# Optimization experiments

Hardware: AMD Instinct MI355X
Metric: run time of the kernel (lower is better)

## Reference

```python
import jax, jax.numpy as jnp
import numpy as np
import math

B, T, D = 1, 4096, 1024
H = 16
HD = D // H  # 64


def _rotate_half(x):
    d = x.shape[-1] // 2
    return jnp.concatenate([-x[..., d:], x[..., :d]], axis=-1)


def setup_inputs() -> dict:
    key = jax.random.key(0)
    k1, k2, k3 = jax.random.split(key, 3)
    x = jax.random.normal(k1, (B, T, D), dtype=jnp.float32)
    # Linear weights stored as (in, out) so forward is x @ W
    w_qkv = jax.random.normal(k2, (D, 3 * D), dtype=jnp.float32) * (1.0 / math.sqrt(D))
    w_proj = jax.random.normal(k3, (D, D), dtype=jnp.float32) * (1.0 / math.sqrt(D))
    return {"x": x, "w_qkv": w_qkv, "w_proj": w_proj}


def reference(x, w_qkv, w_proj):
    b, t, c = x.shape
    qkv = x @ w_qkv  # [b,t,3c]
    q, k, v = jnp.split(qkv, 3, axis=-1)
    # [b,h,t,hd]
    q = q.reshape(b, t, H, HD).transpose(0, 2, 1, 3)
    k = k.reshape(b, t, H, HD).transpose(0, 2, 1, 3)
    v = v.reshape(b, t, H, HD).transpose(0, 2, 1, 3)

    # RoPE (rotate_half style)
    inv_freq = 1.0 / (10000.0 ** (jnp.arange(0, HD, 2, dtype=jnp.float32) / HD))
    pos = jnp.arange(t, dtype=jnp.float32)
    freqs = jnp.outer(pos, inv_freq)            # [t, hd/2]
    cos = jnp.concatenate([jnp.cos(freqs), jnp.cos(freqs)], axis=-1)[None, None]  # [1,1,t,hd]
    sin = jnp.concatenate([jnp.sin(freqs), jnp.sin(freqs)], axis=-1)[None, None]
    q = q * cos + _rotate_half(q) * sin
    k = k * cos + _rotate_half(k) * sin

    att = jnp.einsum('bhqd,bhkd->bhqk', q, k) / math.sqrt(HD)  # [b,h,t,t]
    causal = jnp.tril(jnp.ones((t, t), dtype=bool))
    att = jnp.where(causal, att, -jnp.inf)
    att = jax.nn.softmax(att, axis=-1)
    # dropout is identity in eval mode
    y = jnp.einsum('bhqk,bhkd->bhqd', att, v)
    y = y.transpose(0, 2, 1, 3).reshape(b, t, c)
    return y @ w_proj
```

## Files before the change

kernel.cpp:

```cpp
#include <hip/hip_runtime.h>
#include <math.h>

#define TT 4096
#define DD 1024
#define NH 16
#define HD 64

typedef __attribute__((ext_vector_type(8))) _Float16 half8v;
typedef __attribute__((ext_vector_type(4))) _Float16 half4v;
typedef __attribute__((ext_vector_type(4))) float f32x4;

#define GLDS16(g, l)                                                        \
    __builtin_amdgcn_global_load_lds(                                       \
        (const __attribute__((address_space(1))) void*)(g),                 \
        (__attribute__((address_space(3))) void*)(l), 16, 0, 0)

__global__ __launch_bounds__(256) void cast_x(const float* __restrict__ X,
                                              _Float16* __restrict__ Xh)
{
    const int i = (blockIdx.x * 256 + threadIdx.x) * 8;
    float4 a = *(const float4*)&X[i];
    float4 b = *(const float4*)&X[i + 4];
    half8v o = {(_Float16)a.x, (_Float16)a.y, (_Float16)a.z, (_Float16)a.w,
                (_Float16)b.x, (_Float16)b.y, (_Float16)b.z, (_Float16)b.w};
    *(half8v*)&Xh[i] = o;
}

__global__ __launch_bounds__(256) void transpose_cast(
    const float* __restrict__ W, _Float16* __restrict__ WT, int K, int N)
{
    __shared__ float tile[64][65];
    const int t = threadIdx.x;
    const int k0 = blockIdx.y * 64, n0 = blockIdx.x * 64;
    const int c = (t & 15) * 4, r = t >> 4;
#pragma unroll
    for (int i = 0; i < 4; i++) {
        float4 v = *(const float4*)&W[(size_t)(k0 + r + 16 * i) * N + n0 + c];
        tile[r + 16 * i][c + 0] = v.x;
        tile[r + 16 * i][c + 1] = v.y;
        tile[r + 16 * i][c + 2] = v.z;
        tile[r + 16 * i][c + 3] = v.w;
    }
    __syncthreads();
#pragma unroll
    for (int i = 0; i < 4; i++) {
        const int n = r + 16 * i;
        half4v o;
        o[0] = (_Float16)tile[c + 0][n];
        o[1] = (_Float16)tile[c + 1][n];
        o[2] = (_Float16)tile[c + 2][n];
        o[3] = (_Float16)tile[c + 3][n];
        *(half4v*)&WT[(size_t)(n0 + n) * K + k0 + c] = o;
    }
}

template <int MODE>
__global__ __launch_bounds__(256) void gemm_h(
    const _Float16* __restrict__ A, const _Float16* __restrict__ Bt,
    float* __restrict__ C0, _Float16* __restrict__ Q,
    _Float16* __restrict__ Kk, _Float16* __restrict__ V,
    int M, int N, int K)
{
    __shared__ _Float16 As[128 * 32];
    __shared__ _Float16 Bs[128 * 32];
    const int tid  = threadIdx.x;
    const int wave = tid >> 6;
    const int lane = tid & 63;
    const int quad = lane >> 4;
    const int n16  = lane & 15;
    const int n0 = blockIdx.x * 128;
    const int m0 = blockIdx.y * 128;
    const int wr = (wave & 1) * 64;
    const int wc = (wave >> 1) * 64;

    f32x4 acc[4][4];
#pragma unroll
    for (int i = 0; i < 4; i++)
#pragma unroll
        for (int j = 0; j < 4; j++) acc[i][j] = (f32x4){0.f, 0.f, 0.f, 0.f};

    const int srow = tid >> 2;
    const int scol = (tid & 3) * 8;
    const _Float16* Ag = A + (size_t)(m0 + srow) * K + scol;
    const _Float16* Bg = Bt + (size_t)(n0 + srow) * K + scol;
    _Float16* AsW = As + (size_t)wave * 512;
    _Float16* BsW = Bs + (size_t)wave * 512;

    for (int k0 = 0; k0 < K; k0 += 32) {
        __syncthreads();
        GLDS16(Ag + k0, AsW);
        GLDS16(Ag + (size_t)64 * K + k0, AsW + 2048);
        GLDS16(Bg + k0, BsW);
        GLDS16(Bg + (size_t)64 * K + k0, BsW + 2048);
        __syncthreads();

        half8v aF[4], bF[4];
#pragma unroll
        for (int i = 0; i < 4; i++)
            aF[i] = *(const half8v*)&As[(size_t)(wr + i * 16 + n16) * 32 + quad * 8];
#pragma unroll
        for (int j = 0; j < 4; j++)
            bF[j] = *(const half8v*)&Bs[(size_t)(wc + j * 16 + n16) * 32 + quad * 8];
#pragma unroll
        for (int i = 0; i < 4; i++)
#pragma unroll
            for (int j = 0; j < 4; j++)
                acc[i][j] = __builtin_amdgcn_mfma_f32_16x16x32_f16(
                    aF[i], bF[j], acc[i][j], 0, 0, 0);
    }

#pragma unroll
    for (int i = 0; i < 4; i++) {
#pragma unroll
        for (int j = 0; j < 4; j++) {
#pragma unroll
            for (int r = 0; r < 4; r++) {
                const int m = m0 + wr + i * 16 + quad * 4 + r;
                const int n = n0 + wc + j * 16 + n16;
                const float val = acc[i][j][r];
                if (MODE == 0) {
                    C0[(size_t)m * N + n] = val;
                } else {
                    const int which = n >> 10;
                    const int col = n & 1023;
                    const int h = col >> 6, d = col & 63;
                    const size_t off = ((size_t)h * TT + m) * HD + d;
                    if (which == 0) Q[off] = (_Float16)val;
                    else if (which == 1) Kk[off] = (_Float16)val;
                    else V[off] = (_Float16)val;
                }
            }
        }
    }
}

__global__ __launch_bounds__(256) void rope_h(_Float16* __restrict__ Q,
                                              _Float16* __restrict__ Kb)
{
    const int idx = blockIdx.x * 256 + threadIdx.x;
    const int i = idx & 31;
    const int t = (idx >> 5) & (TT - 1);
    const int h = idx >> 17;
    if (h >= NH) return;

    const float inv = expf(-(float)i * (logf(10000.0f) / 32.0f));
    const float f = (float)t * inv;
    const float c = cosf(f), s = sinf(f);
    const size_t base = ((size_t)h * TT + t) * HD + i;
    const float QS = 0.125f * 1.44269504f;

    float q1 = (float)Q[base], q2 = (float)Q[base + 32];
    Q[base]      = (_Float16)((q1 * c - q2 * s) * QS);
    Q[base + 32] = (_Float16)((q2 * c + q1 * s) * QS);
    float k1 = (float)Kb[base], k2 = (float)Kb[base + 32];
    Kb[base]      = (_Float16)(k1 * c - k2 * s);
    Kb[base + 32] = (_Float16)(k2 * c + k1 * s);
}

__global__ __launch_bounds__(256) void transpose_v(
    const _Float16* __restrict__ V, _Float16* __restrict__ Vt)
{
    __shared__ _Float16 tile[256][72];
    const int h = blockIdx.y;
    const int t0 = blockIdx.x * 256;
    const int tid = threadIdx.x;
    const _Float16* Vg = V + (size_t)h * TT * HD;
    _Float16* Vo = Vt + (size_t)h * TT * HD;

#pragma unroll
    for (int i = 0; i < 4; i++) {
        const int chunk = tid + 256 * i;
        const int row = chunk >> 2, c = (chunk & 3) * 16;
        half8v v0 = *(const half8v*)(Vg + (size_t)(t0 + row) * HD + c);
        half8v v1 = *(const half8v*)(Vg + (size_t)(t0 + row) * HD + c + 8);
        *(half8v*)&tile[row][c] = v0;
        *(half8v*)&tile[row][c + 8] = v1;
    }
    __syncthreads();

    const int s = tid & 15;
#pragma unroll
    for (int dd = 0; dd < 4; ++dd) {
        const int d = dd * 16 + (tid >> 4);
        half8v o0, o1;
#pragma unroll
        for (int e = 0; e < 8; e++) o0[e] = tile[s * 16 + e][d];
#pragma unroll
        for (int e = 0; e < 8; e++) o1[e] = tile[s * 16 + 8 + e][d];
        *(half8v*)(Vo + (size_t)d * TT + t0 + s * 16) = o0;
        *(half8v*)(Vo + (size_t)d * TT + t0 + s * 16 + 8) = o1;
    }
}

__global__ __launch_bounds__(256) void attn_kernel(
    const _Float16* __restrict__ Qh, const _Float16* __restrict__ Kh,
    const _Float16* __restrict__ Vt, _Float16* __restrict__ Y)
{
    __shared__ _Float16 Ks[2][32][32];
    __shared__ _Float16 Vs[64][32];
    __shared__ _Float16 Ps[4][32][32];

    const int tid  = threadIdx.x;
    const int wave = tid >> 6;
    const int lane = tid & 63;
    const int quad = lane >> 4;
    const int n16  = lane & 15;
    const int h  = blockIdx.y;
    const int qt = gridDim.x - 1 - blockIdx.x;
    const int q0 = qt * 128;
    const int rowbase = q0 + wave * 32;

    const _Float16* Qg = Qh + (size_t)h * TT * HD;
    const _Float16* Kg = Kh + (size_t)h * TT * HD;
    const _Float16* Vg = Vt + (size_t)h * TT * HD;

    half8v aQ[2][2];
#pragma unroll
    for (int g = 0; g < 2; g++) {
        const int row = rowbase + g * 16 + n16;
#pragma unroll
        for (int c = 0; c < 2; c++)
            aQ[g][c] = *(const half8v*)(Qg + (size_t)row * HD + c * 32 + quad * 8);
    }

    f32x4 O[2][4];
#pragma unroll
    for (int g = 0; g < 2; g++)
#pragma unroll
        for (int d = 0; d < 4; d++) O[g][d] = (f32x4){0.f, 0.f, 0.f, 0.f};
    float l[2][4] = {{0.f, 0.f, 0.f, 0.f}, {0.f, 0.f, 0.f, 0.f}};

    const int kc = tid >> 7, kj = (tid >> 2) & 31, ks = tid & 3;
    const _Float16* kSrc = Kg + (size_t)kj * HD + kc * 32 + ks * 8;
    const int vd = tid >> 2, vs = tid & 3;
    const _Float16* vSrc = Vg + (size_t)vd * TT + vs * 8;
    _Float16* ksBase = &Ks[0][0][0] + (size_t)wave * 512;
    _Float16* vsBase = &Vs[0][0] + (size_t)wave * 512;

    const int nTiles = qt * 4 + 4;

    for (int it = 0; it < nTiles; ++it) {
        const int j0 = it * 32;
        __syncthreads();
        GLDS16(kSrc + (size_t)j0 * HD, ksBase);
        GLDS16(vSrc + j0, vsBase);
        __syncthreads();

        if (j0 <= rowbase + 31) {
            const bool needMask = (j0 + 31 > rowbase);

            f32x4 S[2][2];
#pragma unroll
            for (int g = 0; g < 2; g++)
#pragma unroll
                for (int st = 0; st < 2; st++) {
                    S[g][st] = (f32x4){0.f, 0.f, 0.f, 0.f};
#pragma unroll
                    for (int c = 0; c < 2; c++) {
                        half8v bK = *(const half8v*)&Ks[c][st * 16 + n16][quad * 8];
                        S[g][st] = __builtin_amdgcn_mfma_f32_16x16x32_f16(
                            aQ[g][c], bK, S[g][st], 0, 0, 0);
                    }
                }

#pragma unroll
            for (int g = 0; g < 2; g++)
#pragma unroll
                for (int r = 0; r < 4; r++) {
                    const int row = rowbase + g * 16 + quad * 4 + r;
                    float x0 = S[g][0][r];
                    float x1 = S[g][1][r];
                    if (needMask) {
                        x0 = (j0 + n16      <= row) ? x0 : -1e30f;
                        x1 = (j0 + 16 + n16 <= row) ? x1 : -1e30f;
                    }
                    const float p0 = __builtin_amdgcn_exp2f(x0);
                    const float p1 = __builtin_amdgcn_exp2f(x1);
                    l[g][r] += p0 + p1;
                    Ps[wave][g * 16 + quad * 4 + r][n16]      = (_Float16)p0;
                    Ps[wave][g * 16 + quad * 4 + r][16 + n16] = (_Float16)p1;
                }

            half8v bV[4];
#pragma unroll
            for (int d = 0; d < 4; d++)
                bV[d] = *(const half8v*)&Vs[d * 16 + n16][quad * 8];
#pragma unroll
            for (int g = 0; g < 2; g++) {
                half8v aP = *(const half8v*)&Ps[wave][g * 16 + n16][quad * 8];
#pragma unroll
                for (int d = 0; d < 4; d++)
                    O[g][d] = __builtin_amdgcn_mfma_f32_16x16x32_f16(
                        aP, bV[d], O[g][d], 0, 0, 0);
            }
        }
    }

#pragma unroll
    for (int g = 0; g < 2; g++)
#pragma unroll
        for (int r = 0; r < 4; r++) {
            float s = l[g][r];
            s += __shfl_xor(s, 1);
            s += __shfl_xor(s, 2);
            s += __shfl_xor(s, 4);
            s += __shfl_xor(s, 8);
            const float inv = 1.0f / s;
            const int row = rowbase + g * 16 + quad * 4 + r;
            _Float16* yrow = Y + (size_t)row * DD + h * HD;
#pragma unroll
            for (int d = 0; d < 4; d++)
                yrow[d * 16 + n16] = (_Float16)(O[g][d][r] * inv);
        }
}

extern "C" void kernel_launch(void* const* d_in, const int* in_sizes, int n_in,
                              void* d_out, int out_size, void* d_ws, size_t ws_size,
                              hipStream_t stream)
{
    const float* x      = (const float*)d_in[0];
    const float* w_qkv  = (const float*)d_in[1];
    const float* w_proj = (const float*)d_in[2];
    float* out = (float*)d_out;

    char* ws = (char*)d_ws;
    const size_t MB = 1u << 20;
    _Float16* xh  = (_Float16*)(ws);
    _Float16* WqT = (_Float16*)(ws + 8 * MB);
    _Float16* WpT = (_Float16*)(ws + 14 * MB);
    _Float16* Qh  = (_Float16*)(ws + 16 * MB);
    _Float16* Kh  = (_Float16*)(ws + 24 * MB);
    _Float16* Vh  = (_Float16*)(ws + 32 * MB);
    _Float16* Vtg = (_Float16*)(ws + 40 * MB);
    _Float16* Yh  = (_Float16*)(ws + 48 * MB);

    dim3 blk(256);

    cast_x<<<(TT * DD) / (256 * 8), blk, 0, stream>>>(x, xh);
    transpose_cast<<<dim3(3072 / 64, DD / 64), blk, 0, stream>>>(w_qkv, WqT, DD, 3 * DD);
    transpose_cast<<<dim3(DD / 64, DD / 64), blk, 0, stream>>>(w_proj, WpT, DD, DD);

    gemm_h<1><<<dim3(3072 / 128, TT / 128), blk, 0, stream>>>(
        xh, WqT, nullptr, Qh, Kh, Vh, TT, 3 * DD, DD);

    rope_h<<<(NH * TT * 32) / 256, blk, 0, stream>>>(Qh, Kh);
    transpose_v<<<dim3(TT / 256, NH), blk, 0, stream>>>(Vh, Vtg);

    attn_kernel<<<dim3(TT / 128, NH), blk, 0, stream>>>(Qh, Kh, Vtg, Yh);

    gemm_h<0><<<dim3(DD / 128, TT / 128), blk, 0, stream>>>(
        Yh, WpT, out, nullptr, nullptr, nullptr, TT, DD, DD);
}
```

Before: 312.1 us.

## Split causal attention over key ranges with atomic partial accumulation and finalize pass

Attention for each query tile is now split across up to four blocks, each covering a contiguous range of key tiles. The split count grows with the tile's causal length, which evens out per-block work and gives the GPU more blocks. Each block atomically adds its unnormalized fp16 output and fp32 row sums into zeroed buffers, and a separate finalize kernel divides by the sums. V is repacked into a per-32-key tile layout with interleaved keys so each tile loads contiguously, and P is written to a padded LDS array as half2 stores. The cost is two extra kernels, atomic traffic, and fp16 accumulation of unnormalized partial outputs, which risks precision loss or overflow.

```diff
diff --git a/kernel.cpp b/kernel.cpp
--- a/kernel.cpp
+++ b/kernel.cpp
@@ -1,4 +1,5 @@
 #include <hip/hip_runtime.h>
+#include <hip/hip_fp16.h>
 #include <math.h>
 
 #define TT 4096
@@ -158,14 +159,13 @@
 }
 
 __global__ __launch_bounds__(256) void transpose_v(
-    const _Float16* __restrict__ V, _Float16* __restrict__ Vt)
+    const _Float16* __restrict__ V, _Float16* __restrict__ Vp)
 {
     __shared__ _Float16 tile[256][72];
     const int h = blockIdx.y;
     const int t0 = blockIdx.x * 256;
     const int tid = threadIdx.x;
     const _Float16* Vg = V + (size_t)h * TT * HD;
-    _Float16* Vo = Vt + (size_t)h * TT * HD;
 
 #pragma unroll
     for (int i = 0; i < 4; i++) {
@@ -178,41 +178,62 @@
     }
     __syncthreads();
 
-    const int s = tid & 15;
-#pragma unroll
-    for (int dd = 0; dd < 4; ++dd) {
-        const int d = dd * 16 + (tid >> 4);
-        half8v o0, o1;
-#pragma unroll
-        for (int e = 0; e < 8; e++) o0[e] = tile[s * 16 + e][d];
-#pragma unroll
-        for (int e = 0; e < 8; e++) o1[e] = tile[s * 16 + 8 + e][d];
-        *(half8v*)(Vo + (size_t)d * TT + t0 + s * 16) = o0;
-        *(half8v*)(Vo + (size_t)d * TT + t0 + s * 16 + 8) = o1;
-    }
+    _Float16* Vo = Vp + ((size_t)h * (TT / 32) + (t0 >> 5)) * 64 * 32;
+#pragma unroll
+    for (int i = 0; i < 8; i++) {
+        const int item = tid + 256 * i;
+        const int cc = (item & 3) * 8;
+        const int d = (item >> 2) & 63;
+        const int kbl = item >> 8;
+        half8v o;
+#pragma unroll
+        for (int e = 0; e < 8; e++) {
+            const int cp = cc + e;
+            const int key = (cp >> 1) + 16 * (cp & 1);
+            o[e] = tile[kbl * 32 + key][d];
+        }
+        *(half8v*)(Vo + ((size_t)kbl * 64 + d) * 32 + cc) = o;
+    }
+}
+
+__global__ __launch_bounds__(256) void zero_acc(float4* __restrict__ O4,
+                                                float4* __restrict__ L4)
+{
+    const int i = blockIdx.x * 256 + threadIdx.x;
+    const float4 z = {0.f, 0.f, 0.f, 0.f};
+    O4[i] = z;
+    if (i < 16384) L4[i] = z;
 }
 
 __global__ __launch_bounds__(256) void attn_kernel(
     const _Float16* __restrict__ Qh, const _Float16* __restrict__ Kh,
-    const _Float16* __restrict__ Vt, _Float16* __restrict__ Y)
+    const _Float16* __restrict__ Vp, _Float16* __restrict__ Oacc,
+    float* __restrict__ Lacc)
 {
     __shared__ _Float16 Ks[2][32][32];
     __shared__ _Float16 Vs[64][32];
-    __shared__ _Float16 Ps[4][32][32];
+    __shared__ _Float16 Ps[4][32][40];
 
     const int tid  = threadIdx.x;
     const int wave = tid >> 6;
     const int lane = tid & 63;
     const int quad = lane >> 4;
     const int n16  = lane & 15;
-    const int h  = blockIdx.y;
-    const int qt = gridDim.x - 1 - blockIdx.x;
+    const int h  = blockIdx.z;
+    const int qt = 31 - blockIdx.y;
+    const int s  = blockIdx.x;
+    const int nT = 4 * qt + 4;
+    const int nS = (qt + 8) >> 3;
+    if (s >= nS) return;
+    const int t_beg = s * nT / nS;
+    const int t_end = (s + 1) * nT / nS;
+
     const int q0 = qt * 128;
     const int rowbase = q0 + wave * 32;
 
     const _Float16* Qg = Qh + (size_t)h * TT * HD;
     const _Float16* Kg = Kh + (size_t)h * TT * HD;
-    const _Float16* Vg = Vt + (size_t)h * TT * HD;
+    const _Float16* Vg = Vp + (size_t)h * (TT / 32) * 64 * 32;
 
     half8v aQ[2][2];
 #pragma unroll
@@ -232,18 +253,15 @@
 
     const int kc = tid >> 7, kj = (tid >> 2) & 31, ks = tid & 3;
     const _Float16* kSrc = Kg + (size_t)kj * HD + kc * 32 + ks * 8;
-    const int vd = tid >> 2, vs = tid & 3;
-    const _Float16* vSrc = Vg + (size_t)vd * TT + vs * 8;
+    const _Float16* vSrc = Vg + (size_t)tid * 8;
     _Float16* ksBase = &Ks[0][0][0] + (size_t)wave * 512;
     _Float16* vsBase = &Vs[0][0] + (size_t)wave * 512;
 
-    const int nTiles = qt * 4 + 4;
-
-    for (int it = 0; it < nTiles; ++it) {
+    for (int it = t_beg; it < t_end; ++it) {
         const int j0 = it * 32;
         __syncthreads();
         GLDS16(kSrc + (size_t)j0 * HD, ksBase);
-        GLDS16(vSrc + j0, vsBase);
+        GLDS16(vSrc + (size_t)it * 2048, vsBase);
         __syncthreads();
 
         if (j0 <= rowbase + 31) {
@@ -277,8 +295,8 @@
                     const float p0 = __builtin_amdgcn_exp2f(x0);
                     const float p1 = __builtin_amdgcn_exp2f(x1);
                     l[g][r] += p0 + p1;
-                    Ps[wave][g * 16 + quad * 4 + r][n16]      = (_Float16)p0;
-                    Ps[wave][g * 16 + quad * 4 + r][16 + n16] = (_Float16)p1;
+                    *(__half2*)&Ps[wave][g * 16 + quad * 4 + r][2 * n16] =
+                        __floats2half2_rn(p0, p1);
                 }
 
             half8v bV[4];
@@ -300,18 +318,42 @@
     for (int g = 0; g < 2; g++)
 #pragma unroll
         for (int r = 0; r < 4; r++) {
-            float s = l[g][r];
-            s += __shfl_xor(s, 1);
-            s += __shfl_xor(s, 2);
-            s += __shfl_xor(s, 4);
-            s += __shfl_xor(s, 8);
-            const float inv = 1.0f / s;
+            float sl = l[g][r];
+            sl += __shfl_xor(sl, 1);
+            sl += __shfl_xor(sl, 2);
+            sl += __shfl_xor(sl, 4);
+            sl += __shfl_xor(sl, 8);
             const int row = rowbase + g * 16 + quad * 4 + r;
-            _Float16* yrow = Y + (size_t)row * DD + h * HD;
-#pragma unroll
-            for (int d = 0; d < 4; d++)
-                yrow[d * 16 + n16] = (_Float16)(O[g][d][r] * inv);
+            if (n16 == 0)
+                unsafeAtomicAdd(&Lacc[h * TT + row], sl);
+#pragma unroll
+            for (int d = 0; d < 4; d++) {
+                float v = O[g][d][r];
+                float vn = __shfl_xor(v, 1);
+                if ((lane & 1) == 0) {
+                    __half2* dst = (__half2*)(Oacc +
+                        ((size_t)h * TT + row) * HD + d * 16 + n16);
+                    unsafeAtomicAdd(dst, __floats2half2_rn(v, vn));
+                }
+            }
         }
+}
+
+__global__ __launch_bounds__(256) void finalize(
+    const _Float16* __restrict__ Oacc, const float* __restrict__ Lacc,
+    _Float16* __restrict__ Y)
+{
+    const int gid = blockIdx.x * 256 + threadIdx.x;
+    const int h = gid >> 15;
+    const int rem = gid & 32767;
+    const int t = rem >> 3;
+    const int c = rem & 7;
+    const float inv = 1.0f / Lacc[h * TT + t];
+    half8v o = *(const half8v*)(Oacc + ((size_t)h * TT + t) * HD + c * 8);
+    half8v y;
+#pragma unroll
+    for (int e = 0; e < 8; e++) y[e] = (_Float16)((float)o[e] * inv);
+    *(half8v*)(Y + (size_t)t * DD + h * HD + c * 8) = y;
 }
 
 extern "C" void kernel_launch(void* const* d_in, const int* in_sizes, int n_in,
@@ -325,14 +367,16 @@
 
     char* ws = (char*)d_ws;
     const size_t MB = 1u << 20;
-    _Float16* xh  = (_Float16*)(ws);
-    _Float16* WqT = (_Float16*)(ws + 8 * MB);
-    _Float16* WpT = (_Float16*)(ws + 14 * MB);
-    _Float16* Qh  = (_Float16*)(ws + 16 * MB);
-    _Float16* Kh  = (_Float16*)(ws + 24 * MB);
-    _Float16* Vh  = (_Float16*)(ws + 32 * MB);
-    _Float16* Vtg = (_Float16*)(ws + 40 * MB);
-    _Float16* Yh  = (_Float16*)(ws + 48 * MB);
+    _Float16* xh   = (_Float16*)(ws);
+    _Float16* WqT  = (_Float16*)(ws + 8 * MB);
+    _Float16* WpT  = (_Float16*)(ws + 14 * MB);
+    _Float16* Qh   = (_Float16*)(ws + 16 * MB);
+    _Float16* Kh   = (_Float16*)(ws + 24 * MB);
+    _Float16* Vh   = (_Float16*)(ws + 32 * MB);
+    _Float16* Vp   = (_Float16*)(ws + 40 * MB);
+    _Float16* Yh   = (_Float16*)(ws + 48 * MB);
+    _Float16* Oacc = (_Float16*)(ws + 56 * MB);
+    float*    Lacc = (float*)(ws + 65 * MB);
 
     dim3 blk(256);
 
@@ -344,9 +388,12 @@
         xh, WqT, nullptr, Qh, Kh, Vh, TT, 3 * DD, DD);
 
     rope_h<<<(NH * TT * 32) / 256, blk, 0, stream>>>(Qh, Kh);
-    transpose_v<<<dim3(TT / 256, NH), blk, 0, stream>>>(Vh, Vtg);
-
-    attn_kernel<<<dim3(TT / 128, NH), blk, 0, stream>>>(Qh, Kh, Vtg, Yh);
+    transpose_v<<<dim3(TT / 256, NH), blk, 0, stream>>>(Vh, Vp);
+    zero_acc<<<2048, blk, 0, stream>>>((float4*)Oacc, (float4*)Lacc);
+
+    attn_kernel<<<dim3(4, 32, NH), blk, 0, stream>>>(Qh, Kh, Vp, Oacc, Lacc);
+
+    finalize<<<2048, blk, 0, stream>>>(Oacc, Lacc, Yh);
 
     gemm_h<0><<<dim3(DD / 128, TT / 128), blk, 0, stream>>>(
         Yh, WpT, out, nullptr, nullptr, nullptr, TT, DD, DD);
```

Result: faster. 281.3 us (-9.9%).
